# Performance work log

Hardware: AMD Instinct MI355X
Metric: run time of the kernel (lower is better)

The kernel has to match this reference:

```python
import jax, jax.numpy as jnp
import numpy as np

B, S, E, H = 2, 2048, 1024, 16
D = E // H  # head_dim = 64
TRIL = D * (D + 1) // 2  # 2080


def setup_inputs() -> dict:
    key = jax.random.key(0)
    ks = jax.random.split(key, 6)
    return {
        "x": jax.random.normal(ks[0], (B, S, E), dtype=jnp.float32),
        "params": jax.random.normal(ks[1], (H, TRIL), dtype=jnp.float32),
        "Wv": jax.random.normal(ks[2], (E, E), dtype=jnp.float32) * 0.02,
        "bv": jax.random.normal(ks[3], (E,), dtype=jnp.float32) * 0.02,
        "Wo": jax.random.normal(ks[4], (E, E), dtype=jnp.float32) * 0.02,
        "bo": jax.random.normal(ks[5], (E,), dtype=jnp.float32) * 0.02,
    }


def reference(x, params, Wv, bv, Wo, bo):
    # x: [B,S,E]; 'symmetry' modification, dropout in eval mode (identity).
    bs, seq_len, emb_dim = x.shape
    d = D
    rows, cols = jnp.tril_indices(d)  # row-major, matches torch.tril_indices
    # Build per-head lower-triangular factor then symmetric PSD Wqk = L @ L^T.
    tril = jnp.zeros((H, d, d), dtype=x.dtype).at[:, rows, cols].set(params)
    Wqk = jnp.einsum('hij,hkj->hik', tril, tril)  # [H,d,d]
    xh = x.reshape(bs, seq_len, H, d)             # [B,S,H,d]
    # scores[b,h,s,t] = x_s^T Wqk_h x_t / sqrt(d)
    t = jnp.einsum('bshd,hde->bshe', xh, Wqk)
    scores = jnp.einsum('bshe,bthe->bhst', t, xh) / jnp.sqrt(jnp.asarray(d, x.dtype))
    attn = jax.nn.softmax(scores, axis=-1)        # [B,H,S,S]
    Vh = (x @ Wv.T + bv).reshape(bs, seq_len, H, d)
    out = jnp.einsum('bhst,bthd->bshd', attn, Vh).reshape(bs, seq_len, emb_dim)
    return out @ Wo.T + bo
```

## Files before the change

### kernel.cpp

```cpp
#include <hip/hip_runtime.h>
#include <math.h>

static constexpr int kB = 2;
static constexpr int kS = 2048;
static constexpr int kE = 1024;
static constexpr int kH = 16;
static constexpr int kD = 64;
static constexpr int kTRIL = 2080;

typedef __attribute__((ext_vector_type(8))) __bf16 bf16x8;
typedef __attribute__((ext_vector_type(8))) _Float16 f16x8;
typedef __attribute__((ext_vector_type(4))) _Float16 f16x4;
typedef __attribute__((ext_vector_type(2))) __fp16 fp16x2;
typedef __attribute__((ext_vector_type(4))) float f32x4;
typedef __attribute__((ext_vector_type(16))) float f32x16;
typedef __attribute__((ext_vector_type(4))) unsigned int u32x4;
typedef __attribute__((ext_vector_type(2))) unsigned int u32x2;

__device__ __forceinline__ void split_f16(float f, _Float16& hi, _Float16& lo) {
    hi = (_Float16)f;
    lo = (_Float16)(f - (float)hi);
}

__device__ __forceinline__ void gload_lds16(const void* g, void* l) {
    __builtin_amdgcn_global_load_lds(
        (const __attribute__((address_space(1))) unsigned int*)g,
        (__attribute__((address_space(3))) unsigned int*)l, 16, 0, 0);
}

__device__ __forceinline__ unsigned pack_f16(float a, float b) {
    fp16x2 p = __builtin_amdgcn_cvt_pkrtz(a, b);
    return __builtin_bit_cast(unsigned, p);
}

__device__ __forceinline__ unsigned partner32(unsigned x, int hi) {
    u32x2 r = __builtin_amdgcn_permlane32_swap(x, x, false, false);
    return hi ? r[0] : r[1];
}
__device__ __forceinline__ float partner32_f(float x, int hi) {
    return __builtin_bit_cast(float, partner32(__builtin_bit_cast(unsigned, x), hi));
}

__device__ __forceinline__ float max3f(float a, float b, float c) {
    return fmaxf(fmaxf(a, b), c);
}

__global__ __launch_bounds__(256) void setup_kernel(
    const float* __restrict__ Wv, const float* __restrict__ Wo,
    const float* __restrict__ x, const float* __restrict__ params,
    _Float16* __restrict__ wvf, _Float16* __restrict__ wof,
    _Float16* __restrict__ xf,
    _Float16* __restrict__ wqkh, _Float16* __restrict__ wqkl)
{
    const int bid = blockIdx.x;
    if (bid < 2048) {
        const int half = bid >> 10;
        const int i = (bid & 1023) * 256 + threadIdx.x;
        const float* src = half ? Wo : Wv;
        _Float16* dst = half ? wof : wvf;
        const float4 v = ((const float4*)src)[i];
        f16x4 o = {(_Float16)v.x, (_Float16)v.y, (_Float16)v.z, (_Float16)v.w};
        ((f16x4*)dst)[i] = o;
        return;
    }
    if (bid < 6144) {
        const int i = (bid - 2048) * 256 + threadIdx.x;
        const float4 v = ((const float4*)x)[i];
        f16x4 o = {(_Float16)v.x, (_Float16)v.y, (_Float16)v.z, (_Float16)v.w};
        ((f16x4*)xf)[i] = o;
        return;
    }
    __shared__ float p[kTRIL];
    const int h = bid - 6144;
    for (int i = threadIdx.x; i < kTRIL; i += 256) p[i] = params[h * kTRIL + i];
    __syncthreads();
    for (int idx = threadIdx.x; idx < kD * kD; idx += 256) {
        const int i = idx >> 6;
        const int j = idx & 63;
        const int m = i < j ? i : j;
        const float* pi = p + (i * (i + 1)) / 2;
        const float* pj = p + (j * (j + 1)) / 2;
        float s = 0.f;
        for (int k = 0; k <= m; ++k) s += pi[k] * pj[k];
        _Float16 a, b;
        split_f16(s, a, b);
        wqkh[h * kD * kD + idx] = a;
        wqkl[h * kD * kD + idx] = b;
    }
}

__global__ __launch_bounds__(256) void mid_kernel(
    const _Float16* __restrict__ xf, const _Float16* __restrict__ wvf,
    const float* __restrict__ bv, _Float16* __restrict__ VtG,
    const _Float16* __restrict__ wqkh, const _Float16* __restrict__ wqkl,
    _Float16* __restrict__ Qhf, _Float16* __restrict__ Qlf)
{
    __shared__ char arena[65536];
    const int tid = threadIdx.x;
    const int w = tid >> 6, l = tid & 63;
    const int srow = 8 * w + (l >> 3);
    const int cpos = l & 7;

    if (blockIdx.x < 256) {
        _Float16 (*Ab)[128 * 64] = (_Float16 (*)[128 * 64])arena;
        _Float16 (*Bb)[128 * 64] = (_Float16 (*)[128 * 64])(arena + 32768);
        const int K_ = kE;
        const int g = l >> 4, lm = l & 15;
        const int wm = w >> 1, wn = w & 1;
        const int bm = (blockIdx.x >> 3) * 128, bn = (blockIdx.x & 7) * 128;

        f32x4 acc[4][4];
#pragma unroll
        for (int i = 0; i < 4; ++i)
#pragma unroll
            for (int j = 0; j < 4; ++j) acc[i][j] = (f32x4){0.f, 0.f, 0.f, 0.f};

        auto stage = [&](int buf, int k0) {
#pragma unroll
            for (int j = 0; j < 4; ++j) {
                const int r = 32 * j + srow;
                const int c = cpos ^ (r & 7);
                gload_lds16(xf + (size_t)(bm + r) * K_ + k0 + c * 8, &Ab[buf][j * 2048 + w * 512]);
                gload_lds16(wvf + (size_t)(bn + r) * K_ + k0 + c * 8, &Bb[buf][j * 2048 + w * 512]);
            }
        };

        stage(0, 0);
        __syncthreads();
        int cur = 0;
        const int NT = K_ / 64;
        for (int t = 0; t < NT; ++t) {
            if (t + 1 < NT) stage(cur ^ 1, 64 * (t + 1));
            f16x8 a[4][2], bf[4][2];
#pragma unroll
            for (int i = 0; i < 4; ++i) {
                const int rA = wm * 64 + i * 16 + lm;
                const int rB = wn * 64 + i * 16 + lm;
#pragma unroll
                for (int ks = 0; ks < 2; ++ks) {
                    a[i][ks]  = *(const f16x8*)&Ab[cur][rA * 64 + (((4 * ks + g) ^ (rA & 7)) * 8)];
                    bf[i][ks] = *(const f16x8*)&Bb[cur][rB * 64 + (((4 * ks + g) ^ (rB & 7)) * 8)];
                }
            }
            __builtin_amdgcn_s_setprio(1);
#pragma unroll
            for (int ks = 0; ks < 2; ++ks)
#pragma unroll
                for (int mi = 0; mi < 4; ++mi)
#pragma unroll
                    for (int ni = 0; ni < 4; ++ni)
                        acc[mi][ni] = __builtin_amdgcn_mfma_f32_16x16x32_f16(
                            a[mi][ks], bf[ni][ks], acc[mi][ni], 0, 0, 0);
            __builtin_amdgcn_s_setprio(0);
            __syncthreads();
            cur ^= 1;
        }

#pragma unroll
        for (int ni = 0; ni < 4; ++ni) {
            const int col = bn + wn * 64 + ni * 16 + lm;
            const float bb = bv[col];
            const int hh = col >> 6, dd = col & 63;
#pragma unroll
            for (int mi = 0; mi < 4; ++mi) {
                const int tok = bm + wm * 64 + mi * 16 + g * 4;
                const int b = tok >> 11, s0 = tok & 2047;
                f16x4 pk;
#pragma unroll
                for (int r = 0; r < 4; ++r) pk[r] = (_Float16)(acc[mi][ni][r] + bb);
                *(f16x4*)(VtG + ((size_t)(b * kH + hh) * kD + dd) * kS + s0) = pk;
            }
        }
    } else {
        _Float16* Wh = (_Float16*)arena;
        _Float16* Wl = (_Float16*)(arena + 8192);
        const int wk = blockIdx.x - 256;
        const int b = wk >> 8;
        const int h = (wk >> 4) & 15;
        const int tg = wk & 15;
        const int hi = l >> 5;
        const int lq = l & 31;

#pragma unroll
        for (int j = 0; j < 2; ++j) {
            const int r = 32 * j + srow;
            const int c = cpos ^ (r & 7);
            gload_lds16(wqkh + (size_t)(h * kD + r) * kD + c * 8, &Wh[j * 2048 + w * 512]);
            gload_lds16(wqkl + (size_t)(h * kD + r) * kD + c * 8, &Wl[j * 2048 + w * 512]);
        }

        const int tok = tg * 128 + 32 * w + lq;
        f16x8 xq[4];
        {
            const size_t xoff = ((size_t)(b * kS + tok)) * kE + h * kD + 8 * hi;
#pragma unroll
            for (int ks = 0; ks < 4; ++ks)
                xq[ks] = *(const f16x8*)(xf + xoff + 16 * ks);
        }
        f32x16 acc[2];
#pragma unroll
        for (int r = 0; r < 16; ++r) { acc[0][r] = 0.f; acc[1][r] = 0.f; }
        __syncthreads();

#pragma unroll
        for (int et = 0; et < 2; ++et) {
            const int r = 32 * et + lq;
            const int rb = r * 64;
            const int rsw = r & 7;
#pragma unroll
            for (int ks = 0; ks < 4; ++ks) {
                const int cd = 2 * ks + hi;
                f16x8 wh = *(const f16x8*)&Wh[rb + ((cd ^ rsw) * 8)];
                f16x8 wl = *(const f16x8*)&Wl[rb + ((cd ^ rsw) * 8)];
                acc[et] = __builtin_amdgcn_mfma_f32_32x32x16_f16(wh, xq[ks], acc[et], 0, 0, 0);
                acc[et] = __builtin_amdgcn_mfma_f32_32x32x16_f16(wl, xq[ks], acc[et], 0, 0, 0);
            }
        }

        const float sc = 0.125f * 1.44269504088896340736f;
        const size_t qbase = ((size_t)(b * kS + tok)) * kE + h * kD;
#pragma unroll
        for (int et = 0; et < 2; ++et)
#pragma unroll
            for (int m = 0; m < 4; ++m) {
                const int e0 = 32 * et + 8 * m + 4 * hi;
                f16x4 hv, lv;
#pragma unroll
                for (int j = 0; j < 4; ++j) {
                    _Float16 a, c;
                    split_f16(acc[et][4 * m + j] * sc, a, c);
                    hv[j] = a; lv[j] = c;
                }
                *(f16x4*)(Qhf + qbase + e0) = hv;
                *(f16x4*)(Qlf + qbase + e0) = lv;
            }
    }
}

__global__ __launch_bounds__(256) void gemm_out(
    const _Float16* __restrict__ A, const _Float16* __restrict__ Bw,
    const float* __restrict__ bias, float* __restrict__ C,
    int M, int N, int K)
{
    __shared__ _Float16 Ab[2][128 * 64];
    __shared__ _Float16 Bb[2][128 * 64];

    const int tid = threadIdx.x;
    const int w = tid >> 6, l = tid & 63;
    const int g = l >> 4, lm = l & 15;
    const int wm = w >> 1, wn = w & 1;
    const int bm = blockIdx.y * 128, bn = blockIdx.x * 128;
    const int srow = 8 * w + (l >> 3);
    const int cp = l & 7;

    f32x4 acc[4][4];
#pragma unroll
    for (int i = 0; i < 4; ++i)
#pragma unroll
        for (int j = 0; j < 4; ++j) acc[i][j] = (f32x4){0.f, 0.f, 0.f, 0.f};

    auto stage = [&](int buf, int k0) {
#pragma unroll
        for (int j = 0; j < 4; ++j) {
            const int r = 32 * j + srow;
            const int c = cp ^ (r & 7);
            gload_lds16(A + (size_t)(bm + r) * K + k0 + c * 8, &Ab[buf][j * 2048 + w * 512]);
            gload_lds16(Bw + (size_t)(bn + r) * K + k0 + c * 8, &Bb[buf][j * 2048 + w * 512]);
        }
    };

    stage(0, 0);
    __syncthreads();
    int cur = 0;
    const int NT = K / 64;
    for (int t = 0; t < NT; ++t) {
        if (t + 1 < NT) stage(cur ^ 1, 64 * (t + 1));
        f16x8 a[4][2], bf[4][2];
#pragma unroll
        for (int i = 0; i < 4; ++i) {
            const int rA = wm * 64 + i * 16 + lm;
            const int rB = wn * 64 + i * 16 + lm;
#pragma unroll
            for (int ks = 0; ks < 2; ++ks) {
                a[i][ks]  = *(const f16x8*)&Ab[cur][rA * 64 + (((4 * ks + g) ^ (rA & 7)) * 8)];
                bf[i][ks] = *(const f16x8*)&Bb[cur][rB * 64 + (((4 * ks + g) ^ (rB & 7)) * 8)];
            }
        }
        __builtin_amdgcn_s_setprio(1);
#pragma unroll
        for (int ks = 0; ks < 2; ++ks)
#pragma unroll
            for (int mi = 0; mi < 4; ++mi)
#pragma unroll
                for (int ni = 0; ni < 4; ++ni)
                    acc[mi][ni] = __builtin_amdgcn_mfma_f32_16x16x32_f16(
                        a[mi][ks], bf[ni][ks], acc[mi][ni], 0, 0, 0);
        __builtin_amdgcn_s_setprio(0);
        __syncthreads();
        cur ^= 1;
    }

    float bv4[4];
#pragma unroll
    for (int ni = 0; ni < 4; ++ni) bv4[ni] = bias[bn + wn * 64 + ni * 16 + lm];
#pragma unroll
    for (int mi = 0; mi < 4; ++mi) {
        const int row0 = bm + wm * 64 + mi * 16 + g * 4;
#pragma unroll
        for (int r = 0; r < 4; ++r) {
            float* crow = C + (size_t)(row0 + r) * N;
#pragma unroll
            for (int ni = 0; ni < 4; ++ni)
                crow[bn + wn * 64 + ni * 16 + lm] = acc[mi][ni][r] + bv4[ni];
        }
    }
}

__global__ __launch_bounds__(256, 2) void flash_attn_mfma(
    const _Float16* __restrict__ Qhf, const _Float16* __restrict__ Qlf,
    const _Float16* __restrict__ xf, const _Float16* __restrict__ VtG,
    _Float16* __restrict__ AO)
{
    __shared__ _Float16 Kf[2][64 * 64];
    __shared__ _Float16 Vts[2][64 * 64];

    const int tid = threadIdx.x;
    const int l = tid & 63;
    const int w = tid >> 6;
    const int hi = l >> 5;
    const int lq = l & 31;

    const int s = blockIdx.x + 16 * blockIdx.y + 256 * blockIdx.z;
    const int wk = (s & 7) * 64 + (s >> 3);
    const int q0 = (wk & 15) * 128;
    const int h = (wk >> 4) & 15;
    const int b = wk >> 8;

    f16x8 qh[4], ql[4];
    {
        const size_t qoff = ((size_t)(b * kS + q0 + 32 * w + lq)) * kE + h * kD + 8 * hi;
#pragma unroll
        for (int ks = 0; ks < 4; ++ks) {
            qh[ks] = *(const f16x8*)(Qhf + qoff + 16 * ks);
            ql[ks] = *(const f16x8*)(Qlf + qoff + 16 * ks);
        }
    }
    f16x8 ones;
#pragma unroll
    for (int j = 0; j < 8; ++j) ones[j] = (_Float16)1.0f;

    f32x16 oacc[2], lacc;
#pragma unroll
    for (int r = 0; r < 16; ++r) { oacc[0][r] = 0.f; oacc[1][r] = 0.f; lacc[r] = 0.f; }
    float mrun = -INFINITY;

    const int srow = 8 * w + (l >> 3);
    const int cpos = l & 7;
    const size_t vthead = ((size_t)(b * kH + h) * kD) * kS;
    const size_t xbase = (size_t)(b * kS) * kE + h * kD;

    int koff[2][4];
    int vo[2][2][2];
#pragma unroll
    for (int kt = 0; kt < 2; ++kt) {
        const int key = 32 * kt + lq;
        const int kr = key * 64, ksw = key & 7;
#pragma unroll
        for (int ks = 0; ks < 4; ++ks)
            koff[kt][ks] = kr + (((2 * ks + hi) ^ ksw) * 8);
    }
#pragma unroll
    for (int dt = 0; dt < 2; ++dt) {
        const int d = 32 * dt + lq;
        const int dr = d * 64, dsw = d & 7;
#pragma unroll
        for (int kt = 0; kt < 2; ++kt) {
            vo[dt][kt][0] = dr + (((4 * kt + hi) ^ dsw) * 8);
            vo[dt][kt][1] = dr + (((4 * kt + 2 + hi) ^ dsw) * 8);
        }
    }

    auto stage = [&](int buf, int k0) {
#pragma unroll
        for (int j = 0; j < 2; ++j) {
            const int r = 32 * j + srow;
            const int c = cpos ^ (r & 7);
            gload_lds16(xf + xbase + (size_t)(k0 + r) * kE + c * 8, &Kf[buf][j * 2048 + w * 512]);
            gload_lds16(VtG + vthead + (size_t)r * kS + k0 + c * 8, &Vts[buf][j * 2048 + w * 512]);
        }
    };

    auto tile_body = [&](int curb) {
        f32x16 sacc[2];
#pragma unroll
        for (int r = 0; r < 16; ++r) { sacc[0][r] = 0.f; sacc[1][r] = 0.f; }
#pragma unroll
        for (int kt = 0; kt < 2; ++kt) {
            __builtin_amdgcn_s_setprio(1);
#pragma unroll
            for (int ks = 0; ks < 4; ++ks) {
                f16x8 kf = *(const f16x8*)&Kf[curb][koff[kt][ks]];
                sacc[kt] = __builtin_amdgcn_mfma_f32_32x32x16_f16(kf, qh[ks], sacc[kt], 0, 0, 0);
                sacc[kt] = __builtin_amdgcn_mfma_f32_32x32x16_f16(kf, ql[ks], sacc[kt], 0, 0, 0);
            }
            __builtin_amdgcn_s_setprio(0);
        }

        float m0 = max3f(max3f(sacc[0][0], sacc[0][1], sacc[0][2]),
                         max3f(sacc[0][3], sacc[0][4], sacc[0][5]),
                         max3f(sacc[0][6], sacc[0][7], sacc[0][8]));
        float m1 = max3f(max3f(sacc[0][9], sacc[0][10], sacc[0][11]),
                         max3f(sacc[0][12], sacc[0][13], sacc[0][14]),
                         sacc[0][15]);
        float m2 = max3f(max3f(sacc[1][0], sacc[1][1], sacc[1][2]),
                         max3f(sacc[1][3], sacc[1][4], sacc[1][5]),
                         max3f(sacc[1][6], sacc[1][7], sacc[1][8]));
        float m3 = max3f(max3f(sacc[1][9], sacc[1][10], sacc[1][11]),
                         max3f(sacc[1][12], sacc[1][13], sacc[1][14]),
                         sacc[1][15]);
        float tmax = max3f(max3f(m0, m1, m2), m3, -INFINITY);
        tmax = fmaxf(tmax, partner32_f(tmax, hi));
        if (__any(tmax > mrun + 14.0f)) {
            const float mnew = fmaxf(mrun, tmax);
            const float alpha = exp2f(mrun - mnew);
            oacc[0] *= alpha;
            oacc[1] *= alpha;
            lacc *= alpha;
            mrun = mnew;
        }

#pragma unroll
        for (int kt = 0; kt < 2; ++kt) {
            unsigned wds[8], pw[8];
#pragma unroll
            for (int i = 0; i < 8; ++i) {
                const float p0 = exp2f(sacc[kt][2 * i] - mrun);
                const float p1 = exp2f(sacc[kt][2 * i + 1] - mrun);
                wds[i] = pack_f16(p0, p1);
            }
#pragma unroll
            for (int i = 0; i < 8; ++i) pw[i] = partner32(wds[i], hi);
            u32x4 f0 = hi ? (u32x4){pw[2], pw[3], wds[2], wds[3]}
                          : (u32x4){wds[0], wds[1], pw[0], pw[1]};
            u32x4 f1 = hi ? (u32x4){pw[6], pw[7], wds[6], wds[7]}
                          : (u32x4){wds[4], wds[5], pw[4], pw[5]};
            f16x8 pf0 = __builtin_bit_cast(f16x8, f0);
            f16x8 pf1 = __builtin_bit_cast(f16x8, f1);
            __builtin_amdgcn_s_setprio(1);
            lacc = __builtin_amdgcn_mfma_f32_32x32x16_f16(ones, pf0, lacc, 0, 0, 0);
            lacc = __builtin_amdgcn_mfma_f32_32x32x16_f16(ones, pf1, lacc, 0, 0, 0);
#pragma unroll
            for (int dt = 0; dt < 2; ++dt) {
                f16x8 v0 = *(const f16x8*)&Vts[curb][vo[dt][kt][0]];
                f16x8 v1 = *(const f16x8*)&Vts[curb][vo[dt][kt][1]];
                oacc[dt] = __builtin_amdgcn_mfma_f32_32x32x16_f16(v0, pf0, oacc[dt], 0, 0, 0);
                oacc[dt] = __builtin_amdgcn_mfma_f32_32x32x16_f16(v1, pf1, oacc[dt], 0, 0, 0);
            }
            __builtin_amdgcn_s_setprio(0);
        }
    };

    stage(0, 0);
    for (int t = 0; t < 32; t += 2) {
        __syncthreads();
        if (t + 1 < 32) stage(1, 64 * (t + 1));
        tile_body(0);
        __syncthreads();
        if (t + 2 < 32) stage(0, 64 * (t + 2));
        tile_body(1);
    }

    const float inv = 1.0f / lacc[0];
    const size_t obase = ((size_t)(b * kS + q0 + 32 * w + lq)) * kE + h * kD;
#pragma unroll
    for (int dt = 0; dt < 2; ++dt)
#pragma unroll
        for (int rr = 0; rr < 4; ++rr) {
            const int d0 = 32 * dt + 8 * rr + 4 * hi;
            f16x4 pk;
#pragma unroll
            for (int j = 0; j < 4; ++j) pk[j] = (_Float16)(oacc[dt][4 * rr + j] * inv);
            *(f16x4*)(AO + obase + d0) = pk;
        }
}

extern "C" void kernel_launch(void* const* d_in, const int* in_sizes, int n_in,
                              void* d_out, int out_size, void* d_ws, size_t ws_size,
                              hipStream_t stream) {
    (void)in_sizes; (void)n_in; (void)out_size; (void)ws_size;
    const float* x      = (const float*)d_in[0];
    const float* params = (const float*)d_in[1];
    const float* Wv     = (const float*)d_in[2];
    const float* bv     = (const float*)d_in[3];
    const float* Wo     = (const float*)d_in[4];
    const float* bo     = (const float*)d_in[5];
    float* out = (float*)d_out;

    const size_t NE = (size_t)kB * kS * kE;
    const size_t NW = (size_t)kE * kE;
    const size_t NQ = (size_t)kH * kD * kD;

    char* ws = (char*)d_ws;
    size_t off = 0;
    _Float16* wqkh = (_Float16*)(ws + off); off += NQ * 2;
    _Float16* wqkl = (_Float16*)(ws + off); off += NQ * 2;
    _Float16* xf   = (_Float16*)(ws + off); off += NE * 2;
    _Float16* wvf  = (_Float16*)(ws + off); off += NW * 2;
    _Float16* wof  = (_Float16*)(ws + off); off += NW * 2;
    _Float16* Qhf  = (_Float16*)(ws + off); off += NE * 2;
    _Float16* Qlf  = (_Float16*)(ws + off); off += NE * 2;
    _Float16* VtG  = (_Float16*)(ws + off); off += NE * 2;
    _Float16* AO   = (_Float16*)(ws + off); off += NE * 2;

    setup_kernel<<<6160, 256, 0, stream>>>(Wv, Wo, x, params, wvf, wof, xf, wqkh, wqkl);
    mid_kernel<<<768, 256, 0, stream>>>(xf, wvf, bv, VtG, wqkh, wqkl, Qhf, Qlf);
    flash_attn_mfma<<<dim3(kS / 128, kH, kB), 256, 0, stream>>>(Qhf, Qlf, xf, VtG, AO);
    gemm_out<<<dim3(kE / 128, (kB * kS) / 128), 256, 0, stream>>>(
        AO, wof, bo, out, kB * kS, kE, kE);
}
```

Before: 139.9 us.

## Software-pipeline QK^T of next tile with softmax/PV of current tile

Restructures the flash-attention loop so the QK^T MFMAs for tile t+1 are issued before the softmax and PV work for tile t, with a triple-buffered V tile in LDS so V data stays valid across the skew. This is meant to overlap matrix-core work with the exp/max/pack VALU work and hide LDS latency. It costs an extra set of score accumulators in registers and one more 8KB V buffer, which may reduce occupancy under the 2-blocks launch bound or cause spills.

```diff
diff --git a/kernel.cpp b/kernel.cpp
--- a/kernel.cpp
+++ b/kernel.cpp
@@ -8,7 +8,6 @@
 static constexpr int kD = 64;
 static constexpr int kTRIL = 2080;
 
-typedef __attribute__((ext_vector_type(8))) __bf16 bf16x8;
 typedef __attribute__((ext_vector_type(8))) _Float16 f16x8;
 typedef __attribute__((ext_vector_type(4))) _Float16 f16x4;
 typedef __attribute__((ext_vector_type(2))) __fp16 fp16x2;
@@ -322,7 +321,7 @@
     _Float16* __restrict__ AO)
 {
     __shared__ _Float16 Kf[2][64 * 64];
-    __shared__ _Float16 Vts[2][64 * 64];
+    __shared__ _Float16 Vts[3 * 64 * 64];
 
     const int tid = threadIdx.x;
     const int l = tid & 63;
@@ -380,18 +379,18 @@
         }
     }
 
-    auto stage = [&](int buf, int k0) {
+    auto stage = [&](int kbuf, int vidx, int k0) {
+        _Float16* vdst = &Vts[vidx * 4096];
 #pragma unroll
         for (int j = 0; j < 2; ++j) {
             const int r = 32 * j + srow;
             const int c = cpos ^ (r & 7);
-            gload_lds16(xf + xbase + (size_t)(k0 + r) * kE + c * 8, &Kf[buf][j * 2048 + w * 512]);
-            gload_lds16(VtG + vthead + (size_t)r * kS + k0 + c * 8, &Vts[buf][j * 2048 + w * 512]);
+            gload_lds16(xf + xbase + (size_t)(k0 + r) * kE + c * 8, &Kf[kbuf][j * 2048 + w * 512]);
+            gload_lds16(VtG + vthead + (size_t)r * kS + k0 + c * 8, &vdst[j * 2048 + w * 512]);
         }
     };
 
-    auto tile_body = [&](int curb) {
-        f32x16 sacc[2];
+    auto qk_tile = [&](const _Float16* kbase, f32x16 (&sacc)[2]) {
 #pragma unroll
         for (int r = 0; r < 16; ++r) { sacc[0][r] = 0.f; sacc[1][r] = 0.f; }
 #pragma unroll
@@ -399,13 +398,16 @@
             __builtin_amdgcn_s_setprio(1);
 #pragma unroll
             for (int ks = 0; ks < 4; ++ks) {
-                f16x8 kf = *(const f16x8*)&Kf[curb][koff[kt][ks]];
+                f16x8 kf = *(const f16x8*)&kbase[koff[kt][ks]];
                 sacc[kt] = __builtin_amdgcn_mfma_f32_32x32x16_f16(kf, qh[ks], sacc[kt], 0, 0, 0);
                 sacc[kt] = __builtin_amdgcn_mfma_f32_32x32x16_f16(kf, ql[ks], sacc[kt], 0, 0, 0);
             }
             __builtin_amdgcn_s_setprio(0);
         }
-
+    };
+
+    auto finish = [&](f32x16 (&sacc)[2], int vidx) {
+        const _Float16* vbase = &Vts[vidx * 4096];
         float m0 = max3f(max3f(sacc[0][0], sacc[0][1], sacc[0][2]),
                          max3f(sacc[0][3], sacc[0][4], sacc[0][5]),
                          max3f(sacc[0][6], sacc[0][7], sacc[0][8]));
@@ -418,7 +420,7 @@
         float m3 = max3f(max3f(sacc[1][9], sacc[1][10], sacc[1][11]),
                          max3f(sacc[1][12], sacc[1][13], sacc[1][14]),
                          sacc[1][15]);
-        float tmax = max3f(max3f(m0, m1, m2), m3, -INFINITY);
+        float tmax = fmaxf(fmaxf(m0, m1), fmaxf(m2, m3));
         tmax = fmaxf(tmax, partner32_f(tmax, hi));
         if (__any(tmax > mrun + 14.0f)) {
             const float mnew = fmaxf(mrun, tmax);
@@ -428,7 +430,6 @@
             lacc *= alpha;
             mrun = mnew;
         }
-
 #pragma unroll
         for (int kt = 0; kt < 2; ++kt) {
             unsigned wds[8], pw[8];
@@ -451,8 +452,8 @@
             lacc = __builtin_amdgcn_mfma_f32_32x32x16_f16(ones, pf1, lacc, 0, 0, 0);
 #pragma unroll
             for (int dt = 0; dt < 2; ++dt) {
-                f16x8 v0 = *(const f16x8*)&Vts[curb][vo[dt][kt][0]];
-                f16x8 v1 = *(const f16x8*)&Vts[curb][vo[dt][kt][1]];
+                f16x8 v0 = *(const f16x8*)&vbase[vo[dt][kt][0]];
+                f16x8 v1 = *(const f16x8*)&vbase[vo[dt][kt][1]];
                 oacc[dt] = __builtin_amdgcn_mfma_f32_32x32x16_f16(v0, pf0, oacc[dt], 0, 0, 0);
                 oacc[dt] = __builtin_amdgcn_mfma_f32_32x32x16_f16(v1, pf1, oacc[dt], 0, 0, 0);
             }
@@ -460,15 +461,28 @@
         }
     };
 
-    stage(0, 0);
-    for (int t = 0; t < 32; t += 2) {
+    f32x16 saccA[2], saccB[2];
+
+    stage(0, 0, 0);
+    __syncthreads();
+    qk_tile(&Kf[0][0], saccA);
+    stage(1, 1, 64);
+
+    for (int t = 1; t <= 29; t += 2) {
         __syncthreads();
-        if (t + 1 < 32) stage(1, 64 * (t + 1));
-        tile_body(0);
+        stage(0, (t + 1) % 3, 64 * (t + 1));
+        qk_tile(&Kf[1][0], saccB);
+        finish(saccA, (t - 1) % 3);
+
         __syncthreads();
-        if (t + 2 < 32) stage(0, 64 * (t + 2));
-        tile_body(1);
-    }
+        if (t + 2 <= 31) stage(1, (t + 2) % 3, 64 * (t + 2));
+        qk_tile(&Kf[0][0], saccA);
+        finish(saccB, t % 3);
+    }
+    __syncthreads();
+    qk_tile(&Kf[1][0], saccB);
+    finish(saccA, 30 % 3);
+    finish(saccB, 31 % 3);
 
     const float inv = 1.0f / lacc[0];
     const size_t obase = ((size_t)(b * kS + q0 + 32 * w + lq)) * kE + h * kD;
```

After: 142.6 us. No clear change (+1.9%).
